# Kernel optimization log

Hardware: AMD Instinct MI355X
Metric: run time of the kernel (lower is better)

The kernel has to match this reference:

```python
import jax, jax.numpy as jnp
import numpy as np
import math

B, NPG, DEG = 100, 500, 12          # graphs, nodes/graph, avg degree
F_IN, H, C = 128, 128, 10
RATIO = 0.5
N = B * NPG
E = N * DEG
K1 = math.ceil(NPG * RATIO)          # 250
K2 = math.ceil(K1 * RATIO)           # 125
K3 = math.ceil(K2 * RATIO)           # 63


def _lin(k, i, o):
    return jax.random.uniform(k, (i, o), jnp.float32, -1.0, 1.0) / np.sqrt(i).astype(np.float32)


def setup_inputs() -> dict:
    key = jax.random.key(0)
    ks = jax.random.split(key, 16)
    x = jax.random.normal(ks[0], (N, F_IN), jnp.float32)
    off = (jnp.arange(B, dtype=jnp.int32) * NPG)[:, None]
    src = (jax.random.randint(ks[1], (B, NPG * DEG), 0, NPG, jnp.int32) + off).reshape(-1)
    dst = (jax.random.randint(ks[2], (B, NPG * DEG), 0, NPG, jnp.int32) + off).reshape(-1)
    edge_index = jnp.stack([src, dst])
    return {
        'x': x, 'edge_index': edge_index,
        'Wl1': _lin(ks[3], F_IN, H), 'bl1': jnp.zeros((H,), jnp.float32), 'Wr1': _lin(ks[4], F_IN, H),
        'Wl2': _lin(ks[5], H, H), 'bl2': jnp.zeros((H,), jnp.float32), 'Wr2': _lin(ks[6], H, H),
        'Wl3': _lin(ks[7], H, H), 'bl3': jnp.zeros((H,), jnp.float32), 'Wr3': _lin(ks[8], H, H),
        'pw1': jax.random.normal(ks[9], (H,), jnp.float32),
        'pw2': jax.random.normal(ks[10], (H,), jnp.float32),
        'pw3': jax.random.normal(ks[11], (H,), jnp.float32),
        'W1': _lin(ks[12], 2 * H, H), 'b1': jnp.zeros((H,), jnp.float32),
        'W2': _lin(ks[13], H, H // 2), 'b2': jnp.zeros((H // 2,), jnp.float32),
        'W3': _lin(ks[14], H // 2, C), 'b3': jnp.zeros((C,), jnp.float32),
    }


def sage_conv(x, src, dst, emask, Wl, bl, Wr, n_nodes):
    # PyG SAGEConv: out_i = lin_l(mean_{j->i} x_j) + lin_r(x_i)
    msg = x[src] * emask[:, None]                                   # [E, d]
    agg = jax.ops.segment_sum(msg, dst, num_segments=n_nodes)
    cnt = jax.ops.segment_sum(emask, dst, num_segments=n_nodes)
    mean = agg / jnp.maximum(cnt, 1.0)[:, None]
    return mean @ Wl + bl + x @ Wr


def topk_pool(x, w, src, dst, emask, n_per, k):
    # TopKPooling: score = tanh(x.w/||w||); keep top-k nodes per graph; x_kept *= score
    score = jnp.tanh((x @ w) / jnp.linalg.norm(w))                  # [B*n_per]
    topv, topi = jax.lax.top_k(score.reshape(B, n_per), k)          # [B, k]
    perm = (topi + (jnp.arange(B, dtype=jnp.int32) * n_per)[:, None]).reshape(-1)
    x_new = x[perm] * topv.reshape(-1)[:, None]                     # [B*k, d]
    mapping = jnp.full((B * n_per,), -1, jnp.int32).at[perm].set(jnp.arange(B * k, dtype=jnp.int32))
    ns, nd = mapping[src], mapping[dst]
    emask_new = emask * ((ns >= 0) & (nd >= 0)).astype(emask.dtype)
    return x_new, jnp.maximum(ns, 0), jnp.maximum(nd, 0), emask_new


def readout(x, k):
    # global_max_pool || global_mean_pool (all graphs have exactly k nodes)
    xr = x.reshape(B, k, H)
    return jnp.concatenate([xr.max(axis=1), xr.mean(axis=1)], axis=1)  # [B, 2H]


def reference(x, edge_index, Wl1, bl1, Wr1, Wl2, bl2, Wr2, Wl3, bl3, Wr3,
              pw1, pw2, pw3, W1, b1, W2, b2, W3, b3):
    src, dst = edge_index[0], edge_index[1]
    emask = jnp.ones((E,), jnp.float32)
    h = jax.nn.relu(sage_conv(x, src, dst, emask, Wl1, bl1, Wr1, N))
    h, src, dst, emask = topk_pool(h, pw1, src, dst, emask, NPG, K1)
    x1 = readout(h, K1)
    h = jax.nn.relu(sage_conv(h, src, dst, emask, Wl2, bl2, Wr2, B * K1))
    h, src, dst, emask = topk_pool(h, pw2, src, dst, emask, K1, K2)
    x2 = readout(h, K2)
    h = jax.nn.relu(sage_conv(h, src, dst, emask, Wl3, bl3, Wr3, B * K2))
    h, src, dst, emask = topk_pool(h, pw3, src, dst, emask, K2, K3)
    x3 = readout(h, K3)
    z = x1 + x2 + x3
    z = jax.nn.relu(z @ W1 + b1)   # dropout is identity in eval mode
    z = jax.nn.relu(z @ W2 + b2)
    return jax.nn.log_softmax(z @ W3 + b3, axis=1)   # pool_loss == 0 for TopKPool
```

## Files before the change

### kernel.cpp

```cpp
#include <hip/hip_runtime.h>
#include <math.h>

#define BG    100
#define NPG   500
#define FD    128
#define EE    600000
#define EPG   6000
#define NN    50000
#define K1    250
#define K2    125
#define K3    63
#define CAP   64

typedef short v8s __attribute__((ext_vector_type(8)));
typedef float v4f __attribute__((ext_vector_type(4)));

__device__ __forceinline__ int swz(int p, int N) {
    int j = p & 7, i = p >> 3;
    int chunk = N >> 3, rem = N & 7;
    int mj = j < rem ? j : rem;
    return j * chunk + mj + i;
}

__device__ __forceinline__ unsigned short f2bf(float f) {
    unsigned int u = __float_as_uint(f);
    unsigned int r = (u + 0x7FFFu + ((u >> 16) & 1u)) >> 16;
    return (unsigned short)r;
}
__device__ __forceinline__ float bf2f(unsigned short b) {
    return __uint_as_float(((unsigned int)b) << 16);
}

__global__ __launch_bounds__(1024) void prep_fill_kernel(
        const int* __restrict__ ei, int* __restrict__ deg, int* __restrict__ col,
        const float* __restrict__ Wl1, const float* __restrict__ Wr1,
        const float* __restrict__ Wl2, const float* __restrict__ Wr2,
        const float* __restrict__ Wl3, const float* __restrict__ Wr3,
        unsigned short* __restrict__ wt_hi, unsigned short* __restrict__ wt_lo) {
    __shared__ int lcnt[NPG];
    int tid = threadIdx.x;
    if (blockIdx.x < BG) {
        int b = swz(blockIdx.x, BG);
        for (int i = tid; i < NPG; i += 1024) lcnt[i] = 0;
        __syncthreads();
        for (int e0 = tid; e0 < EPG; e0 += 1024) {
            int e = b * EPG + e0;
            int d = ei[EE + e];
            int pos = atomicAdd(&lcnt[d - b * NPG], 1);
            if (pos < CAP) col[(long long)d * CAP + pos] = ei[e];
        }
        __syncthreads();
        for (int i = tid; i < NPG; i += 1024) deg[b * NPG + i] = lcnt[i];
    } else {
        int id = (blockIdx.x - BG) * 1024 + tid;
        if (id >= 3 * 256 * 128) return;
        int layer = id >> 15, rem = id & 32767;
        int k = rem >> 7, n = rem & 127;
        const float* Wl = layer == 0 ? Wl1 : (layer == 1 ? Wl2 : Wl3);
        const float* Wr = layer == 0 ? Wr1 : (layer == 1 ? Wr2 : Wr3);
        float w = (k < 128) ? Wl[k * 128 + n] : Wr[(k - 128) * 128 + n];
        unsigned short hi = f2bf(w);
        unsigned short lo = f2bf(w - bf2f(hi));
        long long o = (long long)layer * 32768 + n * 256 + k;
        wt_hi[o] = hi;
        wt_lo[o] = lo;
    }
}

__global__ void gather_agg_kernel(const int* __restrict__ deg, const int* __restrict__ col,
                                  const float* __restrict__ x, float* __restrict__ mean,
                                  int n, int NB) {
    int g = swz(blockIdx.x, NB) * 256 + threadIdx.x;
    int node = g >> 5, sub = g & 31;
    if (node >= n) return;
    int d = deg[node]; if (d > CAP) d = CAP;
    const int* cp = col + (long long)node * CAP;
    float ax = 0.0f, ay = 0.0f, az = 0.0f, aw = 0.0f;
    int j = 0;
    for (; j + 4 <= d; j += 4) {
        int s0 = cp[j], s1 = cp[j + 1], s2 = cp[j + 2], s3 = cp[j + 3];
        float4 v0 = ((const float4*)(x + (long long)s0 * FD))[sub];
        float4 v1 = ((const float4*)(x + (long long)s1 * FD))[sub];
        float4 v2 = ((const float4*)(x + (long long)s2 * FD))[sub];
        float4 v3 = ((const float4*)(x + (long long)s3 * FD))[sub];
        ax += v0.x; ay += v0.y; az += v0.z; aw += v0.w;
        ax += v1.x; ay += v1.y; az += v1.z; aw += v1.w;
        ax += v2.x; ay += v2.y; az += v2.z; aw += v2.w;
        ax += v3.x; ay += v3.y; az += v3.z; aw += v3.w;
    }
    for (; j < d; ++j) {
        float4 v = ((const float4*)(x + (long long)cp[j] * FD))[sub];
        ax += v.x; ay += v.y; az += v.z; aw += v.w;
    }
    float inv = 1.0f / fmaxf((float)d, 1.0f);
    float4 o; o.x = ax * inv; o.y = ay * inv; o.z = az * inv; o.w = aw * inv;
    ((float4*)(mean + (long long)node * FD))[sub] = o;
}

__global__ __launch_bounds__(256) void sage_gemm_mfma_kernel(
        const float* __restrict__ mean, const float* __restrict__ x,
        const unsigned short* __restrict__ wt_hi, const unsigned short* __restrict__ wt_lo,
        const float* __restrict__ bl, const float* __restrict__ pw,
        float* __restrict__ hout, float* __restrict__ score, int M, int NB) {
    __shared__ unsigned short Bh[128 * 40], Bl[128 * 40];
    __shared__ float spart[64 * 16];
    __shared__ float snrmp[16];
    int tid  = threadIdx.x;
    int wave = tid >> 6, lane = tid & 63;
    int quad = lane >> 4, l15 = lane & 15;
    int row0 = swz(blockIdx.x, NB) * 64;

    v4f acc[8];
#pragma unroll
    for (int t = 0; t < 8; t++) acc[t] = (v4f){0.f, 0.f, 0.f, 0.f};

    if (tid < 16) {
        float s = 0.f;
#pragma unroll
        for (int t = 0; t < 8; t++) { float p = pw[t * 16 + tid]; s += p * p; }
        snrmp[tid] = s;
    }

    int growA = row0 + 16 * wave + l15; if (growA > M - 1) growA = M - 1;
    int brow = tid >> 1;
    int bk   = (tid & 1) * 16;

    for (int kt = 0; kt < 8; ++kt) {
        const float* Ab = (kt < 4) ? mean : x;
        const float* ap = Ab + (long long)growA * FD + ((kt < 4) ? kt : kt - 4) * 32 + quad * 8;
        float4 v0 = *(const float4*)(ap);
        float4 v1 = *(const float4*)(ap + 4);
        {
            int klog = kt * 32;
            const uint4* sh = (const uint4*)(wt_hi + (long long)brow * 256 + klog + bk);
            const uint4* sl = (const uint4*)(wt_lo + (long long)brow * 256 + klog + bk);
            uint4 vh0 = sh[0], vh1 = sh[1];
            uint4 vl0 = sl[0], vl1 = sl[1];
            *(uint4*)&Bh[brow * 40 + bk]     = vh0;
            *(uint4*)&Bh[brow * 40 + bk + 8] = vh1;
            *(uint4*)&Bl[brow * 40 + bk]     = vl0;
            *(uint4*)&Bl[brow * 40 + bk + 8] = vl1;
        }
        float f[8] = {v0.x, v0.y, v0.z, v0.w, v1.x, v1.y, v1.z, v1.w};
        v8s a_h, a_l;
#pragma unroll
        for (int q = 0; q < 8; q++) {
            unsigned short hb = f2bf(f[q]);
            a_h[q] = (short)hb;
            a_l[q] = (short)f2bf(f[q] - bf2f(hb));
        }
        __syncthreads();
#pragma unroll
        for (int t = 0; t < 8; t++) {
            v8s b_h = *(const v8s*)&Bh[(t * 16 + l15) * 40 + quad * 8];
            v8s b_l = *(const v8s*)&Bl[(t * 16 + l15) * 40 + quad * 8];
            acc[t] = __builtin_amdgcn_mfma_f32_16x16x32_bf16(a_l, b_h, acc[t], 0, 0, 0);
            acc[t] = __builtin_amdgcn_mfma_f32_16x16x32_bf16(a_h, b_l, acc[t], 0, 0, 0);
            acc[t] = __builtin_amdgcn_mfma_f32_16x16x32_bf16(a_h, b_h, acc[t], 0, 0, 0);
        }
        __syncthreads();
    }

    int rbase = row0 + 16 * wave + quad * 4;
    float part[4] = {0.f, 0.f, 0.f, 0.f};
#pragma unroll
    for (int t = 0; t < 8; t++) {
        int colc = t * 16 + l15;
        float blv = bl[colc];
        float pwv = pw[colc];
#pragma unroll
        for (int reg = 0; reg < 4; reg++) {
            float h = fmaxf(acc[t][reg] + blv, 0.0f);
            part[reg] += h * pwv;
            int grow = rbase + reg;
            if (grow < M) hout[(long long)grow * FD + colc] = h;
        }
    }
#pragma unroll
    for (int reg = 0; reg < 4; reg++)
        spart[(16 * wave + quad * 4 + reg) * 16 + l15] = part[reg];
    __syncthreads();
    if (tid < 64) {
        int grow = row0 + tid;
        if (grow < M) {
            float dot = 0.0f;
#pragma unroll
            for (int i = 0; i < 16; i++) dot += spart[tid * 16 + i];
            float nr = 0.0f;
#pragma unroll
            for (int i = 0; i < 16; i++) nr += snrmp[i];
            score[grow] = tanhf(dot / sqrtf(nr));
        }
    }
}

__global__ __launch_bounds__(1024) void topk_tail_kernel(
        const float* __restrict__ score, const float* __restrict__ hout,
        int n_per, int k, int SN,
        float* __restrict__ xp,
        const int* __restrict__ esrc, const int* __restrict__ edst,
        int* __restrict__ gmap,
        int* __restrict__ next_deg, int* __restrict__ next_col,
        float* __restrict__ z, int mode,
        const float* __restrict__ W1, const float* __restrict__ b1,
        const float* __restrict__ W2, const float* __restrict__ b2,
        const float* __restrict__ W3, const float* __restrict__ b3,
        float* __restrict__ out) {
    __shared__ float skey[512];
    __shared__ int   sidx[512];
    __shared__ unsigned long long spk[512];
    __shared__ int   lmap[512];
    __shared__ int   lcnt[512];
    __shared__ float pmax[1024];
    __shared__ float psum[1024];
    __shared__ float zs[256], t1[128], t2[64], t3[16];
    int tid = threadIdx.x;
    int kind, b;
    if (mode == 2) { kind = 1; b = swz(blockIdx.x, BG); }
    else {
        kind = blockIdx.x >= BG ? 1 : 0;
        b = swz(kind ? blockIdx.x - BG : blockIdx.x, BG);
    }

    for (int i = tid; i < SN; i += 1024) { lmap[i] = -1; lcnt[i] = 0; }

    unsigned long long P = 0ULL;
    if (tid < SN) {
        float keyv; unsigned int idx;
        if (tid < n_per) { keyv = score[b * n_per + tid]; idx = (unsigned int)tid; }
        else             { keyv = -INFINITY;              idx = 0x7fffffffu; }
        unsigned int u = __float_as_uint(keyv);
        u = (u & 0x80000000u) ? ~u : (u | 0x80000000u);
        P = ((unsigned long long)u << 32) | (unsigned long long)(~idx);
    }
    for (int ks = 2; ks <= SN; ks <<= 1) {
        for (int j = ks >> 1; j > 0; j >>= 1) {
            unsigned long long Q;
            if (j >= 64) {
                __syncthreads();
                if (tid < SN) spk[tid] = P;
                __syncthreads();
                Q = (tid < SN) ? spk[tid ^ j] : 0ULL;
            } else {
                Q = __shfl_xor(P, j, 64);
            }
            if (tid < SN) {
                bool keepmax = (((tid & ks) == 0) == ((tid & j) == 0));
                if (keepmax == (Q > P)) P = Q;
            }
        }
    }
    if (tid < SN) {
        unsigned int u  = (unsigned int)(P >> 32);
        unsigned int fb = (u & 0x80000000u) ? (u & 0x7fffffffu) : ~u;
        int iv = (int)(~(unsigned int)P);
        skey[tid] = __uint_as_float(fb);
        sidx[tid] = iv;
        if (tid < k) lmap[iv] = tid;
    }
    __syncthreads();

    if (kind == 0) {
        int kbase = b * k;
        if (mode == 0) {
            int nbase = b * n_per;
            for (int e0 = tid; e0 < EPG; e0 += 1024) {
                int e = b * EPG + e0;
                int ls = lmap[esrc[e] - nbase];
                int ld = lmap[edst[e] - nbase];
                if (ls >= 0 && ld >= 0) {
                    int pos = atomicAdd(&lcnt[ld], 1);
                    if (pos < CAP) next_col[(long long)(kbase + ld) * CAP + pos] = kbase + ls;
                }
            }
            __syncthreads();
            for (int i = tid; i < NPG; i += 1024) {
                int l = lmap[i];
                gmap[nbase + i] = l >= 0 ? kbase + l : -1;
            }
        } else {
            int kb1 = b * n_per;
            for (int e0 = tid; e0 < EPG; e0 += 1024) {
                int e = b * EPG + e0;
                int ws = gmap[esrc[e]];
                int wd = gmap[edst[e]];
                int ls = (ws >= 0) ? lmap[ws - kb1] : -1;
                int ld = (wd >= 0) ? lmap[wd - kb1] : -1;
                if (ls >= 0 && ld >= 0) {
                    int pos = atomicAdd(&lcnt[ld], 1);
                    if (pos < CAP) next_col[(long long)(kbase + ld) * CAP + pos] = kbase + ls;
                }
            }
            __syncthreads();
        }
        for (int i = tid; i < k; i += 1024) next_deg[kbase + i] = lcnt[i];
        return;
    }

    int c = tid & 127, s = tid >> 7;
    float mx = -INFINITY, sm = 0.0f;
    {
        int r = s;
        long long hbase = (long long)b * n_per * FD + c;
        long long xbase = (long long)b * k * FD + c;
        for (; r + 24 < k; r += 32) {
            int i0 = sidx[r], i1 = sidx[r + 8], i2 = sidx[r + 16], i3 = sidx[r + 24];
            float k0 = skey[r], k1 = skey[r + 8], k2 = skey[r + 16], k3 = skey[r + 24];
            float v0 = hout[hbase + (long long)i0 * FD] * k0;
            float v1 = hout[hbase + (long long)i1 * FD] * k1;
            float v2 = hout[hbase + (long long)i2 * FD] * k2;
            float v3 = hout[hbase + (long long)i3 * FD] * k3;
            if (mode != 2) {
                xp[xbase + (long long)(r)      * FD] = v0;
                xp[xbase + (long long)(r + 8)  * FD] = v1;
                xp[xbase + (long long)(r + 16) * FD] = v2;
                xp[xbase + (long long)(r + 24) * FD] = v3;
            }
            mx = fmaxf(mx, v0); sm += v0;
            mx = fmaxf(mx, v1); sm += v1;
            mx = fmaxf(mx, v2); sm += v2;
            mx = fmaxf(mx, v3); sm += v3;
        }
        for (; r < k; r += 8) {
            float v = hout[hbase + (long long)sidx[r] * FD] * skey[r];
            if (mode != 2) xp[xbase + (long long)r * FD] = v;
            mx = fmaxf(mx, v); sm += v;
        }
    }
    pmax[tid] = mx; psum[tid] = sm;
    __syncthreads();
    if (tid < 128) {
        float m = -INFINITY, su = 0.0f;
#pragma unroll
        for (int i = 0; i < 8; i++) {
            m = fmaxf(m, pmax[i * 128 + tid]);
            su += psum[i * 128 + tid];
        }
        float mean = su / (float)k;
        if (mode == 0)      { z[b * 256 + tid] = m;  z[b * 256 + 128 + tid] = mean;  }
        else if (mode == 1) { z[b * 256 + tid] += m; z[b * 256 + 128 + tid] += mean; }
        else {
            zs[tid]       = z[b * 256 + tid] + m;
            zs[128 + tid] = z[b * 256 + 128 + tid] + mean;
        }
    }
    if (mode == 2) {
        __syncthreads();
        if (tid < 128) {
            float a = b1[tid];
            for (int kk = 0; kk < 256; kk++) a += zs[kk] * W1[kk * 128 + tid];
            t1[tid] = fmaxf(a, 0.0f);
        }
        __syncthreads();
        if (tid < 64) {
            float a = b2[tid];
            for (int kk = 0; kk < 128; kk++) a += t1[kk] * W2[kk * 64 + tid];
            t2[tid] = fmaxf(a, 0.0f);
        }
        __syncthreads();
        if (tid < 10) {
            float a = b3[tid];
            for (int kk = 0; kk < 64; kk++) a += t2[kk] * W3[kk * 10 + tid];
            t3[tid] = a;
        }
        __syncthreads();
        if (tid == 0) {
            float m = -INFINITY;
            for (int i = 0; i < 10; i++) m = fmaxf(m, t3[i]);
            float su = 0.0f;
            for (int i = 0; i < 10; i++) su += expf(t3[i] - m);
            float ls = logf(su);
            for (int i = 0; i < 10; i++) out[b * 10 + i] = t3[i] - m - ls;
        }
    }
}

extern "C" void kernel_launch(void* const* d_in, const int* in_sizes, int n_in,
                              void* d_out, int out_size, void* d_ws, size_t ws_size,
                              hipStream_t stream) {
    (void)in_sizes; (void)n_in; (void)out_size; (void)ws_size;
    const float* x   = (const float*)d_in[0];
    const int*   ei  = (const int*)d_in[1];
    const float* Wl1 = (const float*)d_in[2];
    const float* bl1 = (const float*)d_in[3];
    const float* Wr1 = (const float*)d_in[4];
    const float* Wl2 = (const float*)d_in[5];
    const float* bl2 = (const float*)d_in[6];
    const float* Wr2 = (const float*)d_in[7];
    const float* Wl3 = (const float*)d_in[8];
    const float* bl3 = (const float*)d_in[9];
    const float* Wr3 = (const float*)d_in[10];
    const float* pw1 = (const float*)d_in[11];
    const float* pw2 = (const float*)d_in[12];
    const float* pw3 = (const float*)d_in[13];
    const float* W1  = (const float*)d_in[14];
    const float* b1  = (const float*)d_in[15];
    const float* W2  = (const float*)d_in[16];
    const float* b2  = (const float*)d_in[17];
    const float* W3  = (const float*)d_in[18];
    const float* b3  = (const float*)d_in[19];
    float* out = (float*)d_out;

    char* ws = (char*)d_ws;
    size_t off = 0;
    auto alloc = [&](size_t bytes) {
        char* p = ws + off;
        off = (off + bytes + 255) & ~(size_t)255;
        return p;
    };
    float* mean  = (float*)alloc((size_t)NN * FD * 4);
    float* hout  = (float*)alloc((size_t)NN * FD * 4);
    float* xp    = (float*)alloc((size_t)BG * K1 * FD * 4);
    float* sc    = (float*)alloc((size_t)NN * 4);
    int*   gmap  = (int*)  alloc((size_t)NN * 4);
    int*   deg   = (int*)  alloc((size_t)NN * 4);
    int*   colb  = (int*)  alloc((size_t)NN * CAP * 4);
    float* z     = (float*)alloc((size_t)BG * 256 * 4);
    unsigned short* wt_hi = (unsigned short*)alloc((size_t)3 * 32768 * 2);
    unsigned short* wt_lo = (unsigned short*)alloc((size_t)3 * 32768 * 2);

    prep_fill_kernel<<<BG + 96, 1024, 0, stream>>>(ei, deg, colb,
                                                   Wl1, Wr1, Wl2, Wr2, Wl3, Wr3, wt_hi, wt_lo);

    {
        int nb = (NN * 32 + 255) / 256;
        gather_agg_kernel<<<nb, 256, 0, stream>>>(deg, colb, x, mean, NN, nb);
    }
    {
        int nb = (NN + 63) / 64;
        sage_gemm_mfma_kernel<<<nb, 256, 0, stream>>>(mean, x, wt_hi, wt_lo,
                                                      bl1, pw1, hout, sc, NN, nb);
    }
    topk_tail_kernel<<<2 * BG, 1024, 0, stream>>>(sc, hout, NPG, K1, 512, xp,
                                                  ei, ei + EE, gmap, deg, colb,
                                                  z, 0, W1, b1, W2, b2, W3, b3, out);

    const int N2 = BG * K1;
    {
        int nb = (N2 * 32 + 255) / 256;
        gather_agg_kernel<<<nb, 256, 0, stream>>>(deg, colb, xp, mean, N2, nb);
    }
    {
        int nb = (N2 + 63) / 64;
        sage_gemm_mfma_kernel<<<nb, 256, 0, stream>>>(mean, xp, wt_hi + 32768, wt_lo + 32768,
                                                      bl2, pw2, hout, sc, N2, nb);
    }
    topk_tail_kernel<<<2 * BG, 1024, 0, stream>>>(sc, hout, K1, K2, 256, xp,
                                                  ei, ei + EE, gmap, deg, colb,
                                                  z, 1, W1, b1, W2, b2, W3, b3, out);

    const int N3 = BG * K2;
    {
        int nb = (N3 * 32 + 255) / 256;
        gather_agg_kernel<<<nb, 256, 0, stream>>>(deg, colb, xp, mean, N3, nb);
    }
    {
        int nb = (N3 + 63) / 64;
        sage_gemm_mfma_kernel<<<nb, 256, 0, stream>>>(mean, xp, wt_hi + 65536, wt_lo + 65536,
                                                      bl3, pw3, hout, sc, N3, nb);
    }
    topk_tail_kernel<<<BG, 1024, 0, stream>>>(sc, hout, K2, K3, 128, (float*)0,
                                              (const int*)0, (const int*)0, (int*)0,
                                              (int*)0, (int*)0,
                                              z, 2, W1, b1, W2, b2, W3, b3, out);
}
```

Before: 256.2 us.

## Load GEMM weight fragments directly from global memory and unroll gather by 8

The SAGE GEMM kernel no longer stages the split-bf16 weight tiles in LDS with block barriers. Each wave now reads its B fragments straight from global memory, relying on L1/L2 caching of the small weight matrix, which removes the shared-memory traffic and both __syncthreads per k-step. The neighbour gather loop also gains an 8-way unrolled stage so more independent loads are in flight per thread. Risks are redundant global or L2 traffic for the weights across the four waves and higher register pressure from the deeper unroll.

```diff
diff --git a/kernel.cpp b/kernel.cpp
--- a/kernel.cpp
+++ b/kernel.cpp
@@ -77,12 +77,29 @@
     const int* cp = col + (long long)node * CAP;
     float ax = 0.0f, ay = 0.0f, az = 0.0f, aw = 0.0f;
     int j = 0;
+    for (; j + 8 <= d; j += 8) {
+        float4 v0 = ((const float4*)(x + (long long)cp[j]     * FD))[sub];
+        float4 v1 = ((const float4*)(x + (long long)cp[j + 1] * FD))[sub];
+        float4 v2 = ((const float4*)(x + (long long)cp[j + 2] * FD))[sub];
+        float4 v3 = ((const float4*)(x + (long long)cp[j + 3] * FD))[sub];
+        float4 v4 = ((const float4*)(x + (long long)cp[j + 4] * FD))[sub];
+        float4 v5 = ((const float4*)(x + (long long)cp[j + 5] * FD))[sub];
+        float4 v6 = ((const float4*)(x + (long long)cp[j + 6] * FD))[sub];
+        float4 v7 = ((const float4*)(x + (long long)cp[j + 7] * FD))[sub];
+        ax += v0.x; ay += v0.y; az += v0.z; aw += v0.w;
+        ax += v1.x; ay += v1.y; az += v1.z; aw += v1.w;
+        ax += v2.x; ay += v2.y; az += v2.z; aw += v2.w;
+        ax += v3.x; ay += v3.y; az += v3.z; aw += v3.w;
+        ax += v4.x; ay += v4.y; az += v4.z; aw += v4.w;
+        ax += v5.x; ay += v5.y; az += v5.z; aw += v5.w;
+        ax += v6.x; ay += v6.y; az += v6.z; aw += v6.w;
+        ax += v7.x; ay += v7.y; az += v7.z; aw += v7.w;
+    }
     for (; j + 4 <= d; j += 4) {
-        int s0 = cp[j], s1 = cp[j + 1], s2 = cp[j + 2], s3 = cp[j + 3];
-        float4 v0 = ((const float4*)(x + (long long)s0 * FD))[sub];
-        float4 v1 = ((const float4*)(x + (long long)s1 * FD))[sub];
-        float4 v2 = ((const float4*)(x + (long long)s2 * FD))[sub];
-        float4 v3 = ((const float4*)(x + (long long)s3 * FD))[sub];
+        float4 v0 = ((const float4*)(x + (long long)cp[j]     * FD))[sub];
+        float4 v1 = ((const float4*)(x + (long long)cp[j + 1] * FD))[sub];
+        float4 v2 = ((const float4*)(x + (long long)cp[j + 2] * FD))[sub];
+        float4 v3 = ((const float4*)(x + (long long)cp[j + 3] * FD))[sub];
         ax += v0.x; ay += v0.y; az += v0.z; aw += v0.w;
         ax += v1.x; ay += v1.y; az += v1.z; aw += v1.w;
         ax += v2.x; ay += v2.y; az += v2.z; aw += v2.w;
@@ -102,7 +119,6 @@
         const unsigned short* __restrict__ wt_hi, const unsigned short* __restrict__ wt_lo,
         const float* __restrict__ bl, const float* __restrict__ pw,
         float* __restrict__ hout, float* __restrict__ score, int M, int NB) {
-    __shared__ unsigned short Bh[128 * 40], Bl[128 * 40];
     __shared__ float spart[64 * 16];
     __shared__ float snrmp[16];
     int tid  = threadIdx.x;
@@ -122,25 +138,12 @@
     }
 
     int growA = row0 + 16 * wave + l15; if (growA > M - 1) growA = M - 1;
-    int brow = tid >> 1;
-    int bk   = (tid & 1) * 16;
 
     for (int kt = 0; kt < 8; ++kt) {
         const float* Ab = (kt < 4) ? mean : x;
         const float* ap = Ab + (long long)growA * FD + ((kt < 4) ? kt : kt - 4) * 32 + quad * 8;
         float4 v0 = *(const float4*)(ap);
         float4 v1 = *(const float4*)(ap + 4);
-        {
-            int klog = kt * 32;
-            const uint4* sh = (const uint4*)(wt_hi + (long long)brow * 256 + klog + bk);
-            const uint4* sl = (const uint4*)(wt_lo + (long long)brow * 256 + klog + bk);
-            uint4 vh0 = sh[0], vh1 = sh[1];
-            uint4 vl0 = sl[0], vl1 = sl[1];
-            *(uint4*)&Bh[brow * 40 + bk]     = vh0;
-            *(uint4*)&Bh[brow * 40 + bk + 8] = vh1;
-            *(uint4*)&Bl[brow * 40 + bk]     = vl0;
-            *(uint4*)&Bl[brow * 40 + bk + 8] = vl1;
-        }
         float f[8] = {v0.x, v0.y, v0.z, v0.w, v1.x, v1.y, v1.z, v1.w};
         v8s a_h, a_l;
 #pragma unroll
@@ -149,16 +152,15 @@
             a_h[q] = (short)hb;
             a_l[q] = (short)f2bf(f[q] - bf2f(hb));
         }
-        __syncthreads();
 #pragma unroll
         for (int t = 0; t < 8; t++) {
-            v8s b_h = *(const v8s*)&Bh[(t * 16 + l15) * 40 + quad * 8];
-            v8s b_l = *(const v8s*)&Bl[(t * 16 + l15) * 40 + quad * 8];
+            long long boff = (long long)(t * 16 + l15) * 256 + kt * 32 + quad * 8;
+            v8s b_h = *(const v8s*)(wt_hi + boff);
+            v8s b_l = *(const v8s*)(wt_lo + boff);
             acc[t] = __builtin_amdgcn_mfma_f32_16x16x32_bf16(a_l, b_h, acc[t], 0, 0, 0);
             acc[t] = __builtin_amdgcn_mfma_f32_16x16x32_bf16(a_h, b_l, acc[t], 0, 0, 0);
             acc[t] = __builtin_amdgcn_mfma_f32_16x16x32_bf16(a_h, b_h, acc[t], 0, 0, 0);
         }
-        __syncthreads();
     }
 
     int rbase = row0 + 16 * wave + quad * 4;
```

New measurement: 338.7 us. 1.32x slower.
